# Kernel optimization log

Measured on AMD Instinct MI355X. Metric: run time of the kernel, lower is better.

The kernel has to match this reference:

```python
import jax, jax.numpy as jnp
import numpy as np

C = 256
CQK = C // 8  # query/key channel dim from Conv3d(in, in//8, 1)


def setup_inputs() -> dict:
    key = jax.random.key(0)
    ks = jax.random.split(key, 8)
    B, D, H, W = 2, 16, 16, 16
    x = jax.random.normal(ks[0], (B, C, D, H, W), dtype=jnp.float32)
    s = 1.0 / np.sqrt(C)
    q_w = jax.random.normal(ks[1], (CQK, C), dtype=jnp.float32) * s
    q_b = jax.random.normal(ks[2], (CQK,), dtype=jnp.float32) * 0.01
    k_w = jax.random.normal(ks[3], (CQK, C), dtype=jnp.float32) * s
    k_b = jax.random.normal(ks[4], (CQK,), dtype=jnp.float32) * 0.01
    v_w = jax.random.normal(ks[5], (C, C), dtype=jnp.float32) * s
    v_b = jax.random.normal(ks[6], (C,), dtype=jnp.float32) * 0.01
    gamma = jax.random.normal(ks[7], (1,), dtype=jnp.float32)
    return {"x": x, "q_w": q_w, "q_b": q_b, "k_w": k_w, "k_b": k_b,
            "v_w": v_w, "v_b": v_b, "gamma": gamma}


def reference(x, q_w, q_b, k_w, k_b, v_w, v_b, gamma):
    B, Cc, D, H, W = x.shape
    N = D * H * W
    xf = x.reshape(B, Cc, N)  # [B, C, N]
    # 1x1x1 Conv3d == channel-mixing matmul
    q = jnp.einsum('oc,bcn->bon', q_w, xf) + q_b[None, :, None]  # [B, C/8, N]
    k = jnp.einsum('oc,bcn->bon', k_w, xf) + k_b[None, :, None]  # [B, C/8, N]
    v = jnp.einsum('oc,bcn->bon', v_w, xf) + v_b[None, :, None]  # [B, C, N]
    # attention[b, i, j] = sum_c q[b, c, i] * k[b, c, j]
    attn = jnp.einsum('bci,bcj->bij', q, k)  # [B, N, N]
    attn = jax.nn.softmax(attn, axis=-1)
    # out[b, c, i] = sum_j v[b, c, j] * attn[b, i, j]
    out = jnp.einsum('bcj,bij->bci', v, attn)  # [B, C, N]
    out = out.reshape(B, Cc, D, H, W)
    return gamma[0] * out + x
```

## Files before the change

### kernel.cpp

```cpp
#include <hip/hip_runtime.h>

#define C_DIM 256
#define CQK   32
#define N_DIM 4096
#define B_DIM 2

typedef __attribute__((ext_vector_type(8))) short bf16x8;
typedef __attribute__((ext_vector_type(4))) float f32x4;

__device__ __forceinline__ unsigned short f2bf(float f) {
    union { float f; unsigned u; } v; v.f = f;
    unsigned r = v.u + 0x7FFFu + ((v.u >> 16) & 1u);
    return (unsigned short)(r >> 16);
}
__device__ __forceinline__ unsigned pk2(float a, float b) {
    return (unsigned)f2bf(a) | ((unsigned)f2bf(b) << 16);
}
__device__ __forceinline__ unsigned pk2t(float a, float b) {
    union { float f; unsigned u; } ua, ub; ua.f = a; ub.f = b;
    return __builtin_amdgcn_perm(ub.u, ua.u, 0x07060302u);
}
#define EXP2(x) __builtin_amdgcn_exp2f(x)
#define MFMA(A, B, C) __builtin_amdgcn_mfma_f32_16x16x32_bf16((A), (B), (C), 0, 0, 0)

__global__ __launch_bounds__(256) void wconv(
    const float* __restrict__ q_w, const float* __restrict__ q_b,
    const float* __restrict__ k_w, const float* __restrict__ k_b,
    const float* __restrict__ v_w, const float* __restrict__ v_b,
    unsigned short* __restrict__ wbf, float* __restrict__ biasf)
{
    const float LOG2E = 1.4426950408889634f;
    int o = blockIdx.x, c = threadIdx.x;
    float w;
    if (o < 32)       w = q_w[o * C_DIM + c] * LOG2E;
    else if (o < 64)  w = k_w[(o - 32) * C_DIM + c];
    else              w = v_w[(o - 64) * C_DIM + c];
    wbf[o * C_DIM + c] = f2bf(w);
    if (c == 0) biasf[o] = (o < 32) ? q_b[o] * LOG2E
                         : (o < 64) ? k_b[o - 32] : v_b[o - 64];
}

__global__ __launch_bounds__(256, 2) void qkv_proj(
    const float* __restrict__ x, const unsigned short* __restrict__ wbf,
    const float* __restrict__ biasf,
    unsigned short* __restrict__ qT, unsigned short* __restrict__ kT,
    unsigned short* __restrict__ vbf)
{
    __shared__ __align__(16) unsigned short xsT[32 * 264];
    __shared__ __align__(16) unsigned short qkbuf[2][32 * 36];
    __shared__ __align__(16) unsigned short vbb[256 * 36];
    const int t  = threadIdx.x;
    const int b  = blockIdx.x >> 7;
    const int n0 = (blockIdx.x & 127) * 32;

    {
        int n4 = t & 3, cq = t >> 2;
        const float* xp = x + ((size_t)(b * C_DIM + cq * 4)) * N_DIM + n0 + n4 * 8;
        float a0[8], a1[8], a2[8], a3[8];
        *(float4*)(a0)     = *(const float4*)(xp);
        *(float4*)(a0 + 4) = *(const float4*)(xp + 4);
        *(float4*)(a1)     = *(const float4*)(xp + N_DIM);
        *(float4*)(a1 + 4) = *(const float4*)(xp + N_DIM + 4);
        *(float4*)(a2)     = *(const float4*)(xp + 2 * N_DIM);
        *(float4*)(a2 + 4) = *(const float4*)(xp + 2 * N_DIM + 4);
        *(float4*)(a3)     = *(const float4*)(xp + 3 * N_DIM);
        *(float4*)(a3 + 4) = *(const float4*)(xp + 3 * N_DIM + 4);
        #pragma unroll
        for (int k = 0; k < 8; ++k) {
            uint2 pw;
            pw.x = pk2(a0[k], a1[k]);
            pw.y = pk2(a2[k], a3[k]);
            *(uint2*)&xsT[(n4 * 8 + k) * 264 + cq * 4] = pw;
        }
    }
    __syncthreads();

    const int w = t >> 6, lid = t & 63, lr = lid & 15, lq = lid >> 4;
    f32x4 acc[5][2] = {};
    #pragma unroll
    for (int ks = 0; ks < 8; ++ks) {
        bf16x8 xb0 = *(const bf16x8*)&xsT[lr * 264 + ks * 32 + lq * 8];
        bf16x8 xb1 = *(const bf16x8*)&xsT[(16 + lr) * 264 + ks * 32 + lq * 8];
        #pragma unroll
        for (int u = 0; u < 5; ++u) {
            int gm = w * 5 + u;
            bf16x8 af = *(const bf16x8*)&wbf[(gm * 16 + lr) * C_DIM + ks * 32 + lq * 8];
            acc[u][0] = MFMA(af, xb0, acc[u][0]);
            acc[u][1] = MFMA(af, xb1, acc[u][1]);
        }
    }
    #pragma unroll
    for (int u = 0; u < 5; ++u) {
        int gm = w * 5 + u;
        float bv[4];
        *(float4*)bv = *(const float4*)&biasf[gm * 16 + lq * 4];
        #pragma unroll
        for (int nh = 0; nh < 2; ++nh) {
            if (gm >= 4) {
                int vc = (gm - 4) * 16 + lq * 4;
                #pragma unroll
                for (int r = 0; r < 4; ++r)
                    vbb[(vc + r) * 36 + nh * 16 + lr] = f2bf(acc[u][nh][r] + bv[r]);
            } else {
                int sel = gm >> 1, half = gm & 1;
                uint2 pw;
                pw.x = pk2(acc[u][nh][0] + bv[0], acc[u][nh][1] + bv[1]);
                pw.y = pk2(acc[u][nh][2] + bv[2], acc[u][nh][3] + bv[3]);
                *(uint2*)&qkbuf[sel][(nh * 16 + lr) * 36 + half * 16 + lq * 4] = pw;
            }
        }
    }
    __syncthreads();
    {
        int sel = t >> 7, idx = t & 127;
        int n = idx >> 2, ch8 = (idx & 3) * 8;
        const unsigned short* src = &qkbuf[sel][n * 36 + ch8];
        uint2 a = *(const uint2*)src;
        uint2 c = *(const uint2*)(src + 4);
        unsigned short* dst = (sel ? kT : qT) + ((size_t)b * N_DIM + n0 + n) * CQK + ch8;
        uint4 st; st.x = a.x; st.y = a.y; st.z = c.x; st.w = c.y;
        *(uint4*)dst = st;
    }
    {
        const unsigned short* src = &vbb[t * 36];
        uint2 a = *(const uint2*)(src + 0);
        uint2 bq = *(const uint2*)(src + 4);
        uint2 c = *(const uint2*)(src + 8);
        uint2 d = *(const uint2*)(src + 12);
        uint2 e = *(const uint2*)(src + 16);
        uint2 f = *(const uint2*)(src + 20);
        uint2 g = *(const uint2*)(src + 24);
        uint2 h = *(const uint2*)(src + 28);
        unsigned short* dst = vbf +
            (((size_t)(b * 4 + (t >> 6)) * 128 + (n0 >> 5)) * 64 + (t & 63)) * 32;
        uint4 s0; s0.x = a.x; s0.y = a.y; s0.z = bq.x; s0.w = bq.y;
        uint4 s1; s1.x = c.x; s1.y = c.y; s1.z = d.x; s1.w = d.y;
        uint4 s2; s2.x = e.x; s2.y = e.y; s2.z = f.x; s2.w = f.y;
        uint4 s3; s3.x = g.x; s3.y = g.y; s3.z = h.x; s3.w = h.y;
        *(uint4*)(dst)      = s0;
        *(uint4*)(dst + 8)  = s1;
        *(uint4*)(dst + 16) = s2;
        *(uint4*)(dst + 24) = s3;
    }
}

__global__ __launch_bounds__(256, 2) void attn_kernel(
    const unsigned short* __restrict__ qT, const unsigned short* __restrict__ kT,
    const unsigned short* __restrict__ vbf, const float* __restrict__ x,
    const float* __restrict__ gamma, float* __restrict__ out)
{
    __shared__ __align__(16) char smem[65536 + 1536];
    char* pbase = smem;
    float* obuf = (float*)smem;
    float* lbuf = (float*)(smem + 65536);

    const int t  = threadIdx.x;
    const int b  = blockIdx.x >> 8;
    const int qt = (blockIdx.x >> 2) & 63;
    const int cs = blockIdx.x & 3;
    const int i0 = qt * 64;
    const int w = t >> 6, lid = t & 63, lr = lid & 15, lq = lid >> 4;

    const unsigned short* qTb = qT + (size_t)b * N_DIM * CQK;
    const unsigned short* kTb = kT + (size_t)b * N_DIM * CQK;
    const unsigned short* vtb = vbf + (size_t)(b * 4 + cs) * 128 * 2048;

    const int pmask = (lr & 7) << 4;
    const int wcol0 = (lq * 8) ^ pmask;
    const int wcol1 = (32 + lq * 8) ^ pmask;
    const int rcol  = (lq * 16) ^ pmask;
    char* pW0 = pbase + (w * 2 + 0) * (64 * 128) + lr * 128;
    char* pW1 = pbase + (w * 2 + 1) * (64 * 128) + lr * 128;

    bf16x8 bq[4];
    #pragma unroll
    for (int it = 0; it < 4; ++it)
        bq[it] = *(const bf16x8*)&qTb[(i0 + it * 16 + lr) * CQK + lq * 8];

    f32x4 oa[4][4] = {};
    float lp[4] = {};

    const int jwbase = w * 1024;
    const int vlane = lr * 32 + lq * 8;

    bf16x8 akc0 = *(const bf16x8*)&kTb[(jwbase + lr) * CQK + lq * 8];
    bf16x8 akc1 = *(const bf16x8*)&kTb[(jwbase + 16 + lr) * CQK + lq * 8];
    bf16x8 avU[4];

    {
        const unsigned short* vt0 = vtb + (size_t)(w * 32) * 2048;
        #pragma unroll
        for (int ct = 0; ct < 4; ++ct)
            avU[ct] = *(const bf16x8*)&vt0[ct * 512 + vlane];
        bf16x8 akn0 = *(const bf16x8*)&kTb[(jwbase + 32 + lr) * CQK + lq * 8];
        bf16x8 akn1 = *(const bf16x8*)&kTb[(jwbase + 32 + 16 + lr) * CQK + lq * 8];
        const f32x4 z = {};
        #pragma unroll
        for (int it = 0; it < 4; ++it) {
            f32x4 s0 = MFMA(akc0, bq[it], z);
            f32x4 s1 = MFMA(akc1, bq[it], z);
            float e0 = EXP2(s0[0]), e1 = EXP2(s0[1]), e2 = EXP2(s0[2]), e3 = EXP2(s0[3]);
            float f0 = EXP2(s1[0]), f1 = EXP2(s1[1]), f2 = EXP2(s1[2]), f3 = EXP2(s1[3]);
            lp[it] += ((e0 + e1) + (e2 + e3)) + ((f0 + f1) + (f2 + f3));
            uint2 pw0; pw0.x = pk2t(e0, e1); pw0.y = pk2t(e2, e3);
            uint2 pw1; pw1.x = pk2t(f0, f1); pw1.y = pk2t(f2, f3);
            char* prow = pW0 + it * 16 * 128;
            *(uint2*)(prow + wcol0) = pw0;
            *(uint2*)(prow + wcol1) = pw1;
        }
        akc0 = akn0; akc1 = akn1;
    }

    #pragma unroll 2
    for (int k = 1; k < 32; ++k) {
        const int jn = jwbase + ((k + 1) & 31) * 32;
        const unsigned short* vtk = vtb + (size_t)(w * 32 + k) * 2048;
        bf16x8 avI[4];
        #pragma unroll
        for (int ct = 0; ct < 4; ++ct)
            avI[ct] = *(const bf16x8*)&vtk[ct * 512 + vlane];
        bf16x8 akn0 = *(const bf16x8*)&kTb[(jn + lr) * CQK + lq * 8];
        bf16x8 akn1 = *(const bf16x8*)&kTb[(jn + 16 + lr) * CQK + lq * 8];
        const char* pR = (k & 1) ? pW0 : pW1;
        bf16x8 bp[4];
        #pragma unroll
        for (int it = 0; it < 4; ++it)
            bp[it] = *(const bf16x8*)(pR + it * 16 * 128 + rcol);
        const f32x4 z = {};
        f32x4 s[4][2];
        #pragma unroll
        for (int it = 0; it < 4; ++it) {
            s[it][0] = MFMA(akc0, bq[it], z);
            s[it][1] = MFMA(akc1, bq[it], z);
        }
        #pragma unroll
        for (int it = 0; it < 4; ++it)
            #pragma unroll
            for (int ct = 0; ct < 4; ++ct)
                oa[ct][it] = MFMA(avU[ct], bp[it], oa[ct][it]);
        char* pWc = (k & 1) ? pW1 : pW0;
        #pragma unroll
        for (int it = 0; it < 4; ++it) {
            float e0 = EXP2(s[it][0][0]), e1 = EXP2(s[it][0][1]);
            float e2 = EXP2(s[it][0][2]), e3 = EXP2(s[it][0][3]);
            float f0 = EXP2(s[it][1][0]), f1 = EXP2(s[it][1][1]);
            float f2 = EXP2(s[it][1][2]), f3 = EXP2(s[it][1][3]);
            lp[it] += ((e0 + e1) + (e2 + e3)) + ((f0 + f1) + (f2 + f3));
            uint2 pw0; pw0.x = pk2t(e0, e1); pw0.y = pk2t(e2, e3);
            uint2 pw1; pw1.x = pk2t(f0, f1); pw1.y = pk2t(f2, f3);
            char* prow = pWc + it * 16 * 128;
            *(uint2*)(prow + wcol0) = pw0;
            *(uint2*)(prow + wcol1) = pw1;
        }
        akc0 = akn0; akc1 = akn1;
        #pragma unroll
        for (int ct = 0; ct < 4; ++ct) avU[ct] = avI[ct];
    }

    {
        bf16x8 bp[4];
        #pragma unroll
        for (int it = 0; it < 4; ++it)
            bp[it] = *(const bf16x8*)(pW1 + it * 16 * 128 + rcol);
        #pragma unroll
        for (int it = 0; it < 4; ++it)
            #pragma unroll
            for (int ct = 0; ct < 4; ++ct)
                oa[ct][it] = MFMA(avU[ct], bp[it], oa[ct][it]);
    }

    #pragma unroll
    for (int it = 0; it < 4; ++it) {
        lp[it] += __shfl_xor(lp[it], 16);
        lp[it] += __shfl_xor(lp[it], 32);
    }
    if (lq == 0) {
        #pragma unroll
        for (int it = 0; it < 4; ++it)
            lbuf[w * 64 + it * 16 + lr] = lp[it];
    }
    __syncthreads();

    for (int ph = 0; ph < 4; ++ph) {
        if (w == ph) {
            #pragma unroll
            for (int ct = 0; ct < 4; ++ct)
                #pragma unroll
                for (int it = 0; it < 4; ++it)
                    #pragma unroll
                    for (int r = 0; r < 4; ++r) {
                        int addr = (ct * 16 + lq * 4 + r) * 68 + it * 16 + lr;
                        if (ph == 0) obuf[addr]  = oa[ct][it][r];
                        else         obuf[addr] += oa[ct][it][r];
                    }
        }
        __syncthreads();
    }
    if (t < 64) {
        float l = lbuf[t] + lbuf[64 + t] + lbuf[128 + t] + lbuf[192 + t];
        lbuf[256 + t] = 1.f / l;
    }
    __syncthreads();

    const float g2 = gamma[0];
    const int c0 = cs * 64;
    const int cc = t >> 2;
    const int ic = (t & 3) * 16;
    const size_t rowbase = ((size_t)b * C_DIM + c0 + cc) * N_DIM + i0 + ic;
    #pragma unroll
    for (int k = 0; k < 4; ++k) {
        float4 ov4 = *(const float4*)&obuf[cc * 68 + ic + k * 4];
        float4 li  = *(const float4*)&lbuf[256 + ic + k * 4];
        float4 xv  = *(const float4*)(x + rowbase + k * 4);
        float4 ov;
        ov.x = g2 * ov4.x * li.x + xv.x;
        ov.y = g2 * ov4.y * li.y + xv.y;
        ov.z = g2 * ov4.z * li.z + xv.z;
        ov.w = g2 * ov4.w * li.w + xv.w;
        *(float4*)(out + rowbase + k * 4) = ov;
    }
}

extern "C" void kernel_launch(void* const* d_in, const int* in_sizes, int n_in,
                              void* d_out, int out_size, void* d_ws, size_t ws_size,
                              hipStream_t stream) {
    const float* x     = (const float*)d_in[0];
    const float* q_w   = (const float*)d_in[1];
    const float* q_b   = (const float*)d_in[2];
    const float* k_w   = (const float*)d_in[3];
    const float* k_b   = (const float*)d_in[4];
    const float* v_w   = (const float*)d_in[5];
    const float* v_b   = (const float*)d_in[6];
    const float* gamma = (const float*)d_in[7];
    float* out = (float*)d_out;

    char* ws = (char*)d_ws;
    unsigned short* qT    = (unsigned short*)(ws);
    unsigned short* kT    = (unsigned short*)(ws + 524288);
    unsigned short* vbf   = (unsigned short*)(ws + 1048576);
    unsigned short* wbf   = (unsigned short*)(ws + 5242880);
    float*          biasf = (float*)(ws + 5406720);

    hipLaunchKernelGGL(wconv, dim3(320), dim3(256), 0, stream,
                       q_w, q_b, k_w, k_b, v_w, v_b, wbf, biasf);
    hipLaunchKernelGGL(qkv_proj, dim3(B_DIM * 128), dim3(256), 0, stream,
                       x, wbf, biasf, qT, kT, vbf);
    hipLaunchKernelGGL(attn_kernel, dim3(B_DIM * 64 * 4), dim3(256), 0, stream,
                       qT, kT, vbf, x, gamma, out);
}
```

Baseline: 118.2 us.

## Enlarge attention query tile to 128 with 512-thread blocks and interleaved MFMA

Each attention block now covers 128 queries with 8 waves, and each wave handles 512 keys instead of 1024. Every V tile and K fragment loaded is therefore reused across twice as many queries, halving V/K global traffic per output. The inner loop also interleaves the QK MFMAs, PV MFMAs and exp/pack for each query sub-tile, which cuts register pressure from the larger accumulator set. In exchange, the 128KB of LDS limits residency to one block per CU, there are only 256 blocks, the cross-wave output reduction now runs as 8 serial phases, and the 128 accumulator floats per lane may spill.

```diff
diff --git a/kernel.cpp b/kernel.cpp
--- a/kernel.cpp
+++ b/kernel.cpp
@@ -144,43 +144,43 @@
     }
 }
 
-__global__ __launch_bounds__(256, 2) void attn_kernel(
+__global__ __launch_bounds__(512, 2) void attn_kernel(
     const unsigned short* __restrict__ qT, const unsigned short* __restrict__ kT,
     const unsigned short* __restrict__ vbf, const float* __restrict__ x,
     const float* __restrict__ gamma, float* __restrict__ out)
 {
-    __shared__ __align__(16) char smem[65536 + 1536];
+    __shared__ __align__(16) char smem[131072];
     char* pbase = smem;
     float* obuf = (float*)smem;
-    float* lbuf = (float*)(smem + 65536);
+    float* lbuf = (float*)(smem + 33792);
 
     const int t  = threadIdx.x;
-    const int b  = blockIdx.x >> 8;
-    const int qt = (blockIdx.x >> 2) & 63;
+    const int b  = blockIdx.x >> 7;
+    const int qt = (blockIdx.x >> 2) & 31;
     const int cs = blockIdx.x & 3;
-    const int i0 = qt * 64;
+    const int i0 = qt * 128;
     const int w = t >> 6, lid = t & 63, lr = lid & 15, lq = lid >> 4;
 
     const unsigned short* qTb = qT + (size_t)b * N_DIM * CQK;
     const unsigned short* kTb = kT + (size_t)b * N_DIM * CQK;
     const unsigned short* vtb = vbf + (size_t)(b * 4 + cs) * 128 * 2048;
 
-    const int pmask = (lr & 7) << 4;
+    const int pmask = (lr & 3) << 4;
     const int wcol0 = (lq * 8) ^ pmask;
     const int wcol1 = (32 + lq * 8) ^ pmask;
     const int rcol  = (lq * 16) ^ pmask;
-    char* pW0 = pbase + (w * 2 + 0) * (64 * 128) + lr * 128;
-    char* pW1 = pbase + (w * 2 + 1) * (64 * 128) + lr * 128;
-
-    bf16x8 bq[4];
-    #pragma unroll
-    for (int it = 0; it < 4; ++it)
+    char* pW0 = pbase + (w * 2 + 0) * 8192 + lr * 64;
+    char* pW1 = pbase + (w * 2 + 1) * 8192 + lr * 64;
+
+    bf16x8 bq[8];
+    #pragma unroll
+    for (int it = 0; it < 8; ++it)
         bq[it] = *(const bf16x8*)&qTb[(i0 + it * 16 + lr) * CQK + lq * 8];
 
-    f32x4 oa[4][4] = {};
-    float lp[4] = {};
-
-    const int jwbase = w * 1024;
+    f32x4 oa[4][8] = {};
+    float lp[8] = {};
+
+    const int jwbase = w * 512;
     const int vlane = lr * 32 + lq * 8;
 
     bf16x8 akc0 = *(const bf16x8*)&kTb[(jwbase + lr) * CQK + lq * 8];
@@ -188,7 +188,7 @@
     bf16x8 avU[4];
 
     {
-        const unsigned short* vt0 = vtb + (size_t)(w * 32) * 2048;
+        const unsigned short* vt0 = vtb + (size_t)(w * 16) * 2048;
         #pragma unroll
         for (int ct = 0; ct < 4; ++ct)
             avU[ct] = *(const bf16x8*)&vt0[ct * 512 + vlane];
@@ -196,7 +196,7 @@
         bf16x8 akn1 = *(const bf16x8*)&kTb[(jwbase + 32 + 16 + lr) * CQK + lq * 8];
         const f32x4 z = {};
         #pragma unroll
-        for (int it = 0; it < 4; ++it) {
+        for (int it = 0; it < 8; ++it) {
             f32x4 s0 = MFMA(akc0, bq[it], z);
             f32x4 s1 = MFMA(akc1, bq[it], z);
             float e0 = EXP2(s0[0]), e1 = EXP2(s0[1]), e2 = EXP2(s0[2]), e3 = EXP2(s0[3]);
@@ -204,7 +204,7 @@
             lp[it] += ((e0 + e1) + (e2 + e3)) + ((f0 + f1) + (f2 + f3));
             uint2 pw0; pw0.x = pk2t(e0, e1); pw0.y = pk2t(e2, e3);
             uint2 pw1; pw1.x = pk2t(f0, f1); pw1.y = pk2t(f2, f3);
-            char* prow = pW0 + it * 16 * 128;
+            char* prow = pW0 + it * 1024;
             *(uint2*)(prow + wcol0) = pw0;
             *(uint2*)(prow + wcol1) = pw1;
         }
@@ -212,9 +212,9 @@
     }
 
     #pragma unroll 2
-    for (int k = 1; k < 32; ++k) {
-        const int jn = jwbase + ((k + 1) & 31) * 32;
-        const unsigned short* vtk = vtb + (size_t)(w * 32 + k) * 2048;
+    for (int k = 1; k < 16; ++k) {
+        const int jn = jwbase + ((k + 1) & 15) * 32;
+        const unsigned short* vtk = vtb + (size_t)(w * 16 + k) * 2048;
         bf16x8 avI[4];
         #pragma unroll
         for (int ct = 0; ct < 4; ++ct)
@@ -222,33 +222,22 @@
         bf16x8 akn0 = *(const bf16x8*)&kTb[(jn + lr) * CQK + lq * 8];
         bf16x8 akn1 = *(const bf16x8*)&kTb[(jn + 16 + lr) * CQK + lq * 8];
         const char* pR = (k & 1) ? pW0 : pW1;
-        bf16x8 bp[4];
-        #pragma unroll
-        for (int it = 0; it < 4; ++it)
-            bp[it] = *(const bf16x8*)(pR + it * 16 * 128 + rcol);
+        char* pWc      = (k & 1) ? pW1 : pW0;
         const f32x4 z = {};
-        f32x4 s[4][2];
-        #pragma unroll
-        for (int it = 0; it < 4; ++it) {
-            s[it][0] = MFMA(akc0, bq[it], z);
-            s[it][1] = MFMA(akc1, bq[it], z);
-        }
-        #pragma unroll
-        for (int it = 0; it < 4; ++it)
+        #pragma unroll
+        for (int it = 0; it < 8; ++it) {
+            bf16x8 bp = *(const bf16x8*)(pR + it * 1024 + rcol);
+            f32x4 s0 = MFMA(akc0, bq[it], z);
+            f32x4 s1 = MFMA(akc1, bq[it], z);
             #pragma unroll
             for (int ct = 0; ct < 4; ++ct)
-                oa[ct][it] = MFMA(avU[ct], bp[it], oa[ct][it]);
-        char* pWc = (k & 1) ? pW1 : pW0;
-        #pragma unroll
-        for (int it = 0; it < 4; ++it) {
-            float e0 = EXP2(s[it][0][0]), e1 = EXP2(s[it][0][1]);
-            float e2 = EXP2(s[it][0][2]), e3 = EXP2(s[it][0][3]);
-            float f0 = EXP2(s[it][1][0]), f1 = EXP2(s[it][1][1]);
-            float f2 = EXP2(s[it][1][2]), f3 = EXP2(s[it][1][3]);
+                oa[ct][it] = MFMA(avU[ct], bp, oa[ct][it]);
+            float e0 = EXP2(s0[0]), e1 = EXP2(s0[1]), e2 = EXP2(s0[2]), e3 = EXP2(s0[3]);
+            float f0 = EXP2(s1[0]), f1 = EXP2(s1[1]), f2 = EXP2(s1[2]), f3 = EXP2(s1[3]);
             lp[it] += ((e0 + e1) + (e2 + e3)) + ((f0 + f1) + (f2 + f3));
             uint2 pw0; pw0.x = pk2t(e0, e1); pw0.y = pk2t(e2, e3);
             uint2 pw1; pw1.x = pk2t(f0, f1); pw1.y = pk2t(f2, f3);
-            char* prow = pWc + it * 16 * 128;
+            char* prow = pWc + it * 1024;
             *(uint2*)(prow + wcol0) = pw0;
             *(uint2*)(prow + wcol1) = pw1;
         }
@@ -258,59 +247,59 @@
     }
 
     {
-        bf16x8 bp[4];
-        #pragma unroll
-        for (int it = 0; it < 4; ++it)
-            bp[it] = *(const bf16x8*)(pW1 + it * 16 * 128 + rcol);
-        #pragma unroll
-        for (int it = 0; it < 4; ++it)
+        #pragma unroll
+        for (int it = 0; it < 8; ++it) {
+            bf16x8 bp = *(const bf16x8*)(pW1 + it * 1024 + rcol);
             #pragma unroll
             for (int ct = 0; ct < 4; ++ct)
-                oa[ct][it] = MFMA(avU[ct], bp[it], oa[ct][it]);
-    }
-
-    #pragma unroll
-    for (int it = 0; it < 4; ++it) {
+                oa[ct][it] = MFMA(avU[ct], bp, oa[ct][it]);
+        }
+    }
+
+    #pragma unroll
+    for (int it = 0; it < 8; ++it) {
         lp[it] += __shfl_xor(lp[it], 16);
         lp[it] += __shfl_xor(lp[it], 32);
     }
+    __syncthreads();
     if (lq == 0) {
         #pragma unroll
-        for (int it = 0; it < 4; ++it)
-            lbuf[w * 64 + it * 16 + lr] = lp[it];
-    }
-    __syncthreads();
-
-    for (int ph = 0; ph < 4; ++ph) {
+        for (int it = 0; it < 8; ++it)
+            lbuf[w * 128 + it * 16 + lr] = lp[it];
+    }
+
+    for (int ph = 0; ph < 8; ++ph) {
         if (w == ph) {
             #pragma unroll
             for (int ct = 0; ct < 4; ++ct)
                 #pragma unroll
-                for (int it = 0; it < 4; ++it)
+                for (int it = 0; it < 8; ++it)
                     #pragma unroll
                     for (int r = 0; r < 4; ++r) {
-                        int addr = (ct * 16 + lq * 4 + r) * 68 + it * 16 + lr;
+                        int addr = (ct * 16 + lq * 4 + r) * 132 + it * 16 + lr;
                         if (ph == 0) obuf[addr]  = oa[ct][it][r];
                         else         obuf[addr] += oa[ct][it][r];
                     }
         }
         __syncthreads();
     }
-    if (t < 64) {
-        float l = lbuf[t] + lbuf[64 + t] + lbuf[128 + t] + lbuf[192 + t];
-        lbuf[256 + t] = 1.f / l;
+    if (t < 128) {
+        float l = 0.f;
+        #pragma unroll
+        for (int ww = 0; ww < 8; ++ww) l += lbuf[ww * 128 + t];
+        lbuf[1024 + t] = 1.f / l;
     }
     __syncthreads();
 
     const float g2 = gamma[0];
     const int c0 = cs * 64;
-    const int cc = t >> 2;
-    const int ic = (t & 3) * 16;
+    const int cc = t >> 3;
+    const int ic = (t & 7) * 16;
     const size_t rowbase = ((size_t)b * C_DIM + c0 + cc) * N_DIM + i0 + ic;
     #pragma unroll
     for (int k = 0; k < 4; ++k) {
-        float4 ov4 = *(const float4*)&obuf[cc * 68 + ic + k * 4];
-        float4 li  = *(const float4*)&lbuf[256 + ic + k * 4];
+        float4 ov4 = *(const float4*)&obuf[cc * 132 + ic + k * 4];
+        float4 li  = *(const float4*)&lbuf[1024 + ic + k * 4];
         float4 xv  = *(const float4*)(x + rowbase + k * 4);
         float4 ov;
         ov.x = g2 * ov4.x * li.x + xv.x;
@@ -345,6 +334,6 @@
                        q_w, q_b, k_w, k_b, v_w, v_b, wbf, biasf);
     hipLaunchKernelGGL(qkv_proj, dim3(B_DIM * 128), dim3(256), 0, stream,
                        x, wbf, biasf, qT, kT, vbf);
-    hipLaunchKernelGGL(attn_kernel, dim3(B_DIM * 64 * 4), dim3(256), 0, stream,
+    hipLaunchKernelGGL(attn_kernel, dim3(B_DIM * 32 * 4), dim3(512), 0, stream,
                        qT, kT, vbf, x, gamma, out);
 }
```

New measurement: 207.2 us. +75.3%, slower.
